# Kernel tuning notes

Hardware: AMD Instinct MI355X
Metric: run time of the kernel (lower is better)

## Reference

```python
import jax, jax.numpy as jnp
import numpy as np

K = 8            # top-k experts per token
GUMBEL_TAU = 1.0 # training-time gumbel noise scale
ROUTER_TEMP = 1.0
SELECT_TEMP = None  # None -> use ROUTER_TEMP for selection
NORM_PROBS = True
T, D, E = 16384, 4096, 128


def setup_inputs() -> dict:
    key = jax.random.key(0)
    k1, k2 = jax.random.split(key)
    h = jax.random.normal(k1, (T, D), dtype=jnp.float32)
    W = jax.random.normal(k2, (D, E), dtype=jnp.float32) * 0.02  # linear gate params
    token_mask = jnp.ones((T,), dtype=bool)
    return {"h": h, "W": W, "token_mask": token_mask}


def reference(h, W, token_mask):
    # compute_logits: linear gate [T,d] @ [d,E] -> [T,E]
    logits_clean = jnp.einsum('td,de->te', h, W)

    t_sel = SELECT_TEMP if SELECT_TEMP is not None else ROUTER_TEMP
    logits_sel = logits_clean / jnp.maximum(t_sel, 1e-06)

    # training path: add gumbel noise (inference=False, gumbel_tau > 0)
    k_gumbel = jax.random.fold_in(jax.random.key(7), 1)
    uniform = jax.random.uniform(k_gumbel, logits_sel.shape, minval=1e-06, maxval=1 - 1e-06)
    gumbel = -jnp.log(-jnp.log(uniform))
    logits_sel = logits_sel + GUMBEL_TAU * gumbel

    logits_sel = jnp.where(token_mask[:, None], logits_sel, -jnp.inf)

    _, top_indices = jax.lax.top_k(logits_sel, K)  # [T, K]
    mask_full = jax.nn.one_hot(top_indices, E).sum(axis=1).astype(bool)  # [T, E]
    mask_full = mask_full & token_mask[:, None]

    t_mix = jnp.maximum(ROUTER_TEMP, 1e-06)
    probs = jax.nn.softmax(logits_clean / t_mix, axis=-1)
    probs = jnp.where(token_mask[:, None], probs, 0.0)

    if NORM_PROBS:
        masked_probs = jnp.where(mask_full, probs, 0.0)
        denom = jnp.maximum(masked_probs.sum(axis=-1, keepdims=True), 1e-09)
        probs = masked_probs / denom
        probs = jnp.where(token_mask[:, None], probs, 0.0)

    return (mask_full, probs, logits_clean, logits_sel)
```

## Files before the change

kernel.cpp:

```cpp
#include <hip/hip_runtime.h>
#include <stdint.h>

#define T_TOK 16384
#define D_DIM 4096
#define E_EXP 128
#define TE ((size_t)T_TOK * E_EXP)

#define TAU 3e-4f
#define FLAG_CAP 8192
#define WT_OFF 65536
#define WT_ELEMS ((size_t)E_EXP * D_DIM)

#define NSPLIT 2
#define KLEN (D_DIM / NSPLIT)
#define BMg 128
#define BKg 64

typedef __attribute__((ext_vector_type(8))) short short8;
typedef __attribute__((ext_vector_type(4))) float f32x4;

#define TF_ROUND(x0, x1, r) { x0 += x1; x1 = (x1 << r) | (x1 >> (32 - r)); x1 ^= x0; }

__host__ __device__ inline void tf2x32(uint32_t k0, uint32_t k1, uint32_t x0, uint32_t x1,
                                       uint32_t* o0, uint32_t* o1) {
  uint32_t ks2 = k0 ^ k1 ^ 0x1BD11BDAu;
  x0 += k0; x1 += k1;
  TF_ROUND(x0, x1, 13) TF_ROUND(x0, x1, 15) TF_ROUND(x0, x1, 26) TF_ROUND(x0, x1, 6)
  x0 += k1; x1 += ks2 + 1u;
  TF_ROUND(x0, x1, 17) TF_ROUND(x0, x1, 29) TF_ROUND(x0, x1, 16) TF_ROUND(x0, x1, 24)
  x0 += ks2; x1 += k0 + 2u;
  TF_ROUND(x0, x1, 13) TF_ROUND(x0, x1, 15) TF_ROUND(x0, x1, 26) TF_ROUND(x0, x1, 6)
  x0 += k0; x1 += k1 + 3u;
  TF_ROUND(x0, x1, 17) TF_ROUND(x0, x1, 29) TF_ROUND(x0, x1, 16) TF_ROUND(x0, x1, 24)
  x0 += k1; x1 += ks2 + 4u;
  TF_ROUND(x0, x1, 13) TF_ROUND(x0, x1, 15) TF_ROUND(x0, x1, 26) TF_ROUND(x0, x1, 6)
  x0 += ks2; x1 += k0 + 5u;
  *o0 = x0; *o1 = x1;
}

__device__ inline uint32_t rng_bits(uint32_t j, uint32_t fk0, uint32_t fk1) {
  uint32_t o0, o1;
  tf2x32(fk0, fk1, 0u, j, &o0, &o1);
  return o0 ^ o1;
}

__device__ inline float gumbel_f32(uint32_t j, uint32_t fk0, uint32_t fk1) {
  uint32_t bits = rng_bits(j, fk0, fk1);
  float f = __uint_as_float((bits >> 9) | 0x3f800000u) - 1.0f;
  const float mn = 1e-6f;
  const float mx = (float)(1.0 - 1e-6);
  float u = fmaxf(mn, f * (mx - mn) + mn);
  float nl = -logf(u);
  return -__logf(nl);
}

__device__ inline double gumbel_f64(uint32_t j, uint32_t fk0, uint32_t fk1) {
  uint32_t bits = rng_bits(j, fk0, fk1);
  float f = __uint_as_float((bits >> 9) | 0x3f800000u) - 1.0f;
  const float mn = 1e-6f;
  const float mx = (float)(1.0 - 1e-6);
  float u = fmaxf(mn, f * (mx - mn) + mn);
  return -log(-log((double)u));
}

__device__ inline unsigned short f2bf(float x) {
  uint32_t u = __float_as_uint(x);
  return (unsigned short)((u + 0x7fffu + ((u >> 16) & 1u)) >> 16);
}
__device__ inline float bf2f(unsigned short h) { return __uint_as_float(((uint32_t)h) << 16); }

__device__ __forceinline__ void gload_lds16(const unsigned short* g, unsigned short* l) {
  __builtin_amdgcn_global_load_lds(
      (const __attribute__((address_space(1))) unsigned int*)g,
      (__attribute__((address_space(3))) unsigned int*)l, 16, 0, 0);
}

__global__ __launch_bounds__(256) void prep_kernel(const float* __restrict__ W,
                                                   unsigned short* __restrict__ WFhi,
                                                   unsigned short* __restrict__ WFlo,
                                                   int* __restrict__ wsi) {
  if (blockIdx.x == 0 && threadIdx.x < 16) wsi[threadIdx.x] = 0;
  const int gslot = blockIdx.x * 256 + threadIdx.x;
  const int kb  = gslot >> 9;
  const int rem = gslot & 511;
  const int cg  = rem >> 6;
  const int ln  = rem & 63;
  const int q = ln >> 4, m = ln & 15;
  const int e  = cg * 16 + m;
  const int k0 = kb * 32 + q * 8;

  __attribute__((aligned(16))) unsigned short hi[8];
  __attribute__((aligned(16))) unsigned short lo[8];
  #pragma unroll
  for (int j = 0; j < 8; j++) {
    float w = W[(size_t)(k0 + j) * E_EXP + e];
    unsigned short h16 = f2bf(w);
    hi[j] = h16;
    lo[j] = f2bf(w - bf2f(h16));
  }
  *(uint4*)(WFhi + (size_t)gslot * 8) = *(const uint4*)hi;
  *(uint4*)(WFlo + (size_t)gslot * 8) = *(const uint4*)lo;
}

__global__ __launch_bounds__(512, 2) void gemm_mfma(const float* __restrict__ h,
                                                    const unsigned short* __restrict__ WFhi,
                                                    const unsigned short* __restrict__ WFlo,
                                                    float* __restrict__ outbase) {
  __shared__ __align__(16) unsigned short sAhi[2][8192];
  __shared__ __align__(16) unsigned short sAlo[2][8192];
  __shared__ __align__(16) unsigned short sBhi[2][8192];
  __shared__ __align__(16) unsigned short sBlo[2][8192];

  const int tid  = threadIdx.x;
  const int ln   = tid & 63;
  const int wv   = tid >> 6;
  const int m    = ln & 15;
  const int quad = ln >> 4;
  const int rh   = wv >> 2;
  const int ch   = wv & 3;
  const int t0   = blockIdx.x * BMg;
  const int kbase = blockIdx.y * KLEN;

  const float* asrc = h + (size_t)(t0 + wv * 16 + m) * D_DIM + kbase + quad * 8;

  const size_t gslot8 = (size_t)tid * 8;
  unsigned short* bdst_h[2][2] = {{ &sBhi[0][wv * 512], &sBhi[0][4096 + wv * 512] },
                                  { &sBhi[1][wv * 512], &sBhi[1][4096 + wv * 512] }};
  unsigned short* bdst_l[2][2] = {{ &sBlo[0][wv * 512], &sBlo[0][4096 + wv * 512] },
                                  { &sBlo[1][wv * 512], &sBlo[1][4096 + wv * 512] }};

  f32x4 acc[4][2];
  #pragma unroll
  for (int r = 0; r < 4; r++)
    #pragma unroll
    for (int c = 0; c < 2; c++) acc[r][c] = (f32x4){0.f, 0.f, 0.f, 0.f};

  {
    const size_t boff = ((size_t)(kbase >> 5)) * 4096;
    gload_lds16(WFhi + boff + gslot8,        bdst_h[0][0]);
    gload_lds16(WFhi + boff + 4096 + gslot8, bdst_h[0][1]);
    gload_lds16(WFlo + boff + gslot8,        bdst_l[0][0]);
    gload_lds16(WFlo + boff + 4096 + gslot8, bdst_l[0][1]);

    float4 a0 = *(const float4*)(asrc);
    float4 a1 = *(const float4*)(asrc + 4);
    float4 a2 = *(const float4*)(asrc + 32);
    float4 a3 = *(const float4*)(asrc + 36);
    float v0[8] = {a0.x, a0.y, a0.z, a0.w, a1.x, a1.y, a1.z, a1.w};
    float v1[8] = {a2.x, a2.y, a2.z, a2.w, a3.x, a3.y, a3.z, a3.w};
    __attribute__((aligned(16))) unsigned short h0[8], l0[8], h1[8], l1[8];
    #pragma unroll
    for (int j = 0; j < 8; j++) {
      unsigned short t16 = f2bf(v0[j]); h0[j] = t16; l0[j] = f2bf(v0[j] - bf2f(t16));
      t16 = f2bf(v1[j]);                h1[j] = t16; l1[j] = f2bf(v1[j] - bf2f(t16));
    }
    *(uint4*)&sAhi[0][(size_t)tid * 8]         = *(const uint4*)h0;
    *(uint4*)&sAlo[0][(size_t)tid * 8]         = *(const uint4*)l0;
    *(uint4*)&sAhi[0][(size_t)(tid + 512) * 8] = *(const uint4*)h1;
    *(uint4*)&sAlo[0][(size_t)(tid + 512) * 8] = *(const uint4*)l1;
    __syncthreads();
  }

  int cur = 0;
  for (int k0 = 0; k0 < KLEN; k0 += BKg) {
    const int kn  = k0 + BKg;
    const bool nxt = (kn < KLEN);
    float4 a0, a1, a2, a3;

    if (nxt) {
      const int nb = cur ^ 1;
      const size_t boff = ((size_t)((kbase + kn) >> 5)) * 4096;
      gload_lds16(WFhi + boff + gslot8,        bdst_h[nb][0]);
      gload_lds16(WFhi + boff + 4096 + gslot8, bdst_h[nb][1]);
      gload_lds16(WFlo + boff + gslot8,        bdst_l[nb][0]);
      gload_lds16(WFlo + boff + 4096 + gslot8, bdst_l[nb][1]);
      a0 = *(const float4*)(asrc + kn);
      a1 = *(const float4*)(asrc + kn + 4);
      a2 = *(const float4*)(asrc + kn + 32);
      a3 = *(const float4*)(asrc + kn + 36);
    }

    short8 ahi[4][2], alo[4][2], bhi[2][2], blo[2][2];
    #pragma unroll
    for (int ks = 0; ks < 2; ks++) {
      #pragma unroll
      for (int r = 0; r < 4; r++) {
        const int slot = (ks * 512 + (rh * 4 + r) * 64 + ln) * 8;
        ahi[r][ks] = *(const short8*)&sAhi[cur][slot];
        alo[r][ks] = *(const short8*)&sAlo[cur][slot];
      }
      #pragma unroll
      for (int c = 0; c < 2; c++) {
        const int slot = (ks * 512 + (ch * 2 + c) * 64 + ln) * 8;
        bhi[c][ks] = *(const short8*)&sBhi[cur][slot];
        blo[c][ks] = *(const short8*)&sBlo[cur][slot];
      }
    }
    #pragma unroll
    for (int ks = 0; ks < 2; ks++)
      #pragma unroll
      for (int r = 0; r < 4; r++)
        #pragma unroll
        for (int c = 0; c < 2; c++) {
          acc[r][c] = __builtin_amdgcn_mfma_f32_16x16x32_bf16(ahi[r][ks], bhi[c][ks], acc[r][c], 0, 0, 0);
          acc[r][c] = __builtin_amdgcn_mfma_f32_16x16x32_bf16(ahi[r][ks], blo[c][ks], acc[r][c], 0, 0, 0);
          acc[r][c] = __builtin_amdgcn_mfma_f32_16x16x32_bf16(alo[r][ks], bhi[c][ks], acc[r][c], 0, 0, 0);
        }

    if (nxt) {
      const int nb = cur ^ 1;
      float v0[8] = {a0.x, a0.y, a0.z, a0.w, a1.x, a1.y, a1.z, a1.w};
      float v1[8] = {a2.x, a2.y, a2.z, a2.w, a3.x, a3.y, a3.z, a3.w};
      __attribute__((aligned(16))) unsigned short h0[8], l0[8], h1[8], l1[8];
      #pragma unroll
      for (int j = 0; j < 8; j++) {
        unsigned short t16 = f2bf(v0[j]); h0[j] = t16; l0[j] = f2bf(v0[j] - bf2f(t16));
        t16 = f2bf(v1[j]);                h1[j] = t16; l1[j] = f2bf(v1[j] - bf2f(t16));
      }
      *(uint4*)&sAhi[nb][(size_t)tid * 8]         = *(const uint4*)h0;
      *(uint4*)&sAlo[nb][(size_t)tid * 8]         = *(const uint4*)l0;
      *(uint4*)&sAhi[nb][(size_t)(tid + 512) * 8] = *(const uint4*)h1;
      *(uint4*)&sAlo[nb][(size_t)(tid + 512) * 8] = *(const uint4*)l1;
    }
    __syncthreads();
    cur ^= 1;
  }

  float* ob = outbase + (size_t)blockIdx.y * TE;
  #pragma unroll
  for (int r = 0; r < 4; r++)
    #pragma unroll
    for (int c = 0; c < 2; c++) {
      const int e = ch * 32 + 16 * c + m;
      #pragma unroll
      for (int reg = 0; reg < 4; reg++) {
        const int t = t0 + rh * 64 + 16 * r + 4 * quad + reg;
        ob[(size_t)t * E_EXP + e] = acc[r][c][reg];
      }
    }
}

__device__ inline uint32_t ordkey(float v) {
  uint32_t b = __float_as_uint(v);
  return (b & 0x80000000u) ? ~b : (b | 0x80000000u);
}
__device__ inline float inv_ordkey(uint32_t k) {
  return (k & 0x80000000u) ? __uint_as_float(k & 0x7fffffffu) : __uint_as_float(~k);
}
__device__ inline uint32_t wave_max_u32(uint32_t v) {
  #pragma unroll
  for (int off = 32; off > 0; off >>= 1) {
    uint32_t o = __shfl_xor(v, off, 64);
    v = (o > v) ? o : v;
  }
  return v;
}
__device__ inline unsigned long long wave_max_u64(unsigned long long v) {
  #pragma unroll
  for (int off = 32; off > 0; off >>= 1) {
    unsigned long long o = __shfl_xor(v, off, 64);
    v = (o > v) ? o : v;
  }
  return v;
}
__device__ inline float wave_max_f32(float v) {
  #pragma unroll
  for (int off = 32; off > 0; off >>= 1) v = fmaxf(v, __shfl_xor(v, off, 64));
  return v;
}
__device__ inline float wave_sum_f32(float v) {
  #pragma unroll
  for (int off = 32; off > 0; off >>= 1) v += __shfl_xor(v, off, 64);
  return v;
}
__device__ inline double wave_sum_f64(double v) {
  #pragma unroll
  for (int off = 32; off > 0; off >>= 1) v += __shfl_xor(v, off, 64);
  return v;
}

__global__ __launch_bounds__(256) void route_kernel(float* out,
                                                    int* flag_cnt, int* flags,
                                                    uint32_t fk0, uint32_t fk1) {
  const int lane = threadIdx.x & 63;
  const int t = blockIdx.x * 4 + (threadIdx.x >> 6);
  const size_t base = (size_t)t * E_EXP;
  float* mask_o   = out;
  float* probs_o  = out + TE;
  float* lclean_o = out + 2 * TE;
  float* lsel_o   = out + 3 * TE;

  double a0 = 0.0, a1 = 0.0;
  #pragma unroll
  for (int s = 0; s < NSPLIT; s++) {
    a0 += (double)out[(size_t)s * TE + base + lane];
    a1 += (double)out[(size_t)s * TE + base + lane + 64];
  }
  const float lc0 = (float)a0, lc1 = (float)a1;

  const float ls0 = lc0 + gumbel_f32((uint32_t)(base + lane), fk0, fk1);
  const float ls1 = lc1 + gumbel_f32((uint32_t)(base + lane + 64), fk0, fk1);

  const uint32_t key0 = ordkey(ls0);
  const uint32_t key1 = ordkey(ls1);
  bool sel0 = false, sel1 = false;
  uint32_t w8 = 0;
  #pragma unroll
  for (int it = 0; it < 8; ++it) {
    uint32_t k0v = sel0 ? 0u : key0;
    uint32_t k1v = sel1 ? 0u : key1;
    w8 = wave_max_u32(k0v > k1v ? k0v : k1v);
    unsigned long long b0 = __ballot(k0v == w8);
    if (b0) {
      if (lane == __ffsll(b0) - 1) sel0 = true;
    } else {
      unsigned long long b1 = __ballot(k1v == w8);
      if (lane == __ffsll(b1) - 1) sel1 = true;
    }
  }
  {
    uint32_t k0v = sel0 ? 0u : key0;
    uint32_t k1v = sel1 ? 0u : key1;
    uint32_t w9 = wave_max_u32(k0v > k1v ? k0v : k1v);
    float gap = inv_ordkey(w8) - inv_ordkey(w9);
    if (lane == 0 && gap < TAU) {
      int idx = atomicAdd(flag_cnt, 1);
      if (idx < FLAG_CAP) flags[idx] = t;
    }
  }

  float mx = wave_max_f32(fmaxf(lc0, lc1));
  float p0 = __expf(lc0 - mx);
  float p1 = __expf(lc1 - mx);
  float s8 = wave_sum_f32((sel0 ? p0 : 0.f) + (sel1 ? p1 : 0.f));

  lclean_o[base + lane]       = lc0;
  lclean_o[base + lane + 64]  = lc1;
  lsel_o[base + lane]         = ls0;
  lsel_o[base + lane + 64]    = ls1;
  mask_o[base + lane]         = sel0 ? 1.0f : 0.0f;
  mask_o[base + lane + 64]    = sel1 ? 1.0f : 0.0f;
  probs_o[base + lane]        = sel0 ? (p0 / s8) : 0.0f;
  probs_o[base + lane + 64]   = sel1 ? (p1 / s8) : 0.0f;
}

__global__ __launch_bounds__(256) void recompute_kernel(const float* __restrict__ h,
                                                        const float* __restrict__ W,
                                                        const int* __restrict__ flag_cnt,
                                                        const int* __restrict__ flags,
                                                        float* __restrict__ mask_out,
                                                        float* __restrict__ probs_out,
                                                        float* __restrict__ lclean_out,
                                                        float* __restrict__ lsel_out,
                                                        uint32_t fk0, uint32_t fk1) {
  __shared__ __align__(16) float shf[D_DIM];
  __shared__ double dsum[E_EXP];
  __shared__ float larr[E_EXP];
  const int tid = threadIdx.x;
  int cnt = *flag_cnt;
  if (cnt > FLAG_CAP) cnt = FLAG_CAP;

  for (int ii = blockIdx.x; ii < cnt; ii += gridDim.x) {
    const int t = flags[ii];
    #pragma unroll
    for (int s = 0; s < 4; s++) {
      int f4 = s * 256 + tid;
      *(float4*)&shf[f4 * 4] = *(const float4*)(h + (size_t)t * D_DIM + f4 * 4);
    }
    __syncthreads();

    const int e = tid & 127;
    const int half = tid >> 7;
    const int kb = half * (D_DIM / 2);
    double acc[8];
    #pragma unroll
    for (int j = 0; j < 8; j++) acc[j] = 0.0;
    #pragma unroll 2
    for (int k = 0; k < D_DIM / 2; k += 8) {
      #pragma unroll
      for (int j = 0; j < 8; j++) {
        int kk = kb + k + j;
        acc[j] = fma((double)shf[kk], (double)W[(size_t)kk * E_EXP + e], acc[j]);
      }
    }
    double a = ((acc[0] + acc[1]) + (acc[2] + acc[3])) + ((acc[4] + acc[5]) + (acc[6] + acc[7]));
    if (half == 1) dsum[e] = a;
    __syncthreads();
    if (half == 0) {
      float lc = (float)(a + dsum[e]);
      larr[e] = lc;
      lclean_out[(size_t)t * E_EXP + e] = lc;
    }
    __syncthreads();

    if (tid < 64) {
      const size_t base = (size_t)t * E_EXP;
      const int lane = tid;
      float lc0 = larr[lane], lc1 = larr[lane + 64];
      float ls0 = lc0 + (float)gumbel_f64((uint32_t)(base + lane), fk0, fk1);
      float ls1 = lc1 + (float)gumbel_f64((uint32_t)(base + lane + 64), fk0, fk1);
      lsel_out[base + lane]      = ls0;
      lsel_out[base + lane + 64] = ls1;

      unsigned long long pk0 = (((unsigned long long)ordkey(ls0)) << 32) | (unsigned)(127 - lane);
      unsigned long long pk1 = (((unsigned long long)ordkey(ls1)) << 32) | (unsigned)(63 - lane);
      bool sel0 = false, sel1 = false;
      #pragma unroll
      for (int it = 0; it < 8; ++it) {
        unsigned long long cc0 = sel0 ? 0ull : pk0;
        unsigned long long cc1 = sel1 ? 0ull : pk1;
        unsigned long long mm = wave_max_u64(cc0 > cc1 ? cc0 : cc1);
        int ew = 127 - (int)(mm & 0xffull);
        if (ew == lane)      sel0 = true;
        if (ew == lane + 64) sel1 = true;
      }
      float mx = wave_max_f32(fmaxf(lc0, lc1));
      double pd0 = exp((double)lc0 - (double)mx);
      double pd1 = exp((double)lc1 - (double)mx);
      double s8 = wave_sum_f64((sel0 ? pd0 : 0.0) + (sel1 ? pd1 : 0.0));

      mask_out[base + lane]       = sel0 ? 1.0f : 0.0f;
      mask_out[base + lane + 64]  = sel1 ? 1.0f : 0.0f;
      probs_out[base + lane]      = sel0 ? (float)(pd0 / s8) : 0.0f;
      probs_out[base + lane + 64] = sel1 ? (float)(pd1 / s8) : 0.0f;
    }
    __syncthreads();
  }
}

extern "C" void kernel_launch(void* const* d_in, const int* in_sizes, int n_in,
                              void* d_out, int out_size, void* d_ws, size_t ws_size,
                              hipStream_t stream) {
  const float* h = (const float*)d_in[0];
  const float* W = (const float*)d_in[1];

  float* out      = (float*)d_out;
  float* mask_o   = out;
  float* probs_o  = out + TE;
  float* lclean_o = out + 2 * TE;
  float* lsel_o   = out + 3 * TE;

  int* wsi   = (int*)d_ws;
  int* flags = wsi + 16;
  unsigned short* WFhi = (unsigned short*)((char*)d_ws + WT_OFF);
  unsigned short* WFlo = WFhi + WT_ELEMS;

  uint32_t fk0, fk1;
  tf2x32(0u, 7u, 0u, 1u, &fk0, &fk1);

  prep_kernel<<<256, 256, 0, stream>>>(W, WFhi, WFlo, wsi);
  gemm_mfma<<<dim3(T_TOK / BMg, NSPLIT), 512, 0, stream>>>(h, WFhi, WFlo, out);
  route_kernel<<<T_TOK / 4, 256, 0, stream>>>(out, wsi, flags, fk0, fk1);
  recompute_kernel<<<256, 256, 0, stream>>>(h, W, wsi, flags, mask_o, probs_o, lclean_o, lsel_o,
                                            fk0, fk1);
}
```

Before: 488.2 us.

## Deepen GEMM pipeline with two-stage A register prefetch and partial waitcnt barriers

Restructures the GEMM main loop into a manually unrolled two-iteration software pipeline. Global loads of A are issued two K-steps ahead into alternating register sets, while B tiles are copied directly into LDS. Barriers use explicit s_waitcnt vmcnt(4) so outstanding A loads can stay in flight across a barrier, and sched_barrier fences keep the compiler from reordering the issue stages. This aims to hide global memory latency behind the MFMA compute, at the cost of more live registers and correctness that depends on the exact count of outstanding loads.

```diff
diff --git a/kernel.cpp b/kernel.cpp
--- a/kernel.cpp
+++ b/kernel.cpp
@@ -102,6 +102,76 @@
   *(uint4*)(WFlo + (size_t)gslot * 8) = *(const uint4*)lo;
 }
 
+#define GEMM_ISSUE_B(KK, NB) do {                                          \
+    const size_t boff_ = ((size_t)((kbase + (KK)) >> 5)) * 4096;           \
+    gload_lds16(WFhi + boff_ + gslot8,        bdst_h[NB][0]);              \
+    gload_lds16(WFhi + boff_ + 4096 + gslot8, bdst_h[NB][1]);              \
+    gload_lds16(WFlo + boff_ + gslot8,        bdst_l[NB][0]);              \
+    gload_lds16(WFlo + boff_ + 4096 + gslot8, bdst_l[NB][1]);              \
+  } while (0)
+
+#define GEMM_LOAD_A(KK, S) do {                                            \
+    S##_0 = *(const float4*)(asrc + (KK));                                 \
+    S##_1 = *(const float4*)(asrc + (KK) + 4);                             \
+    S##_2 = *(const float4*)(asrc + (KK) + 32);                            \
+    S##_3 = *(const float4*)(asrc + (KK) + 36);                            \
+  } while (0)
+
+#define GEMM_CONV_A(S, NB) do {                                            \
+    float v0_[8] = {S##_0.x, S##_0.y, S##_0.z, S##_0.w,                    \
+                    S##_1.x, S##_1.y, S##_1.z, S##_1.w};                   \
+    float v1_[8] = {S##_2.x, S##_2.y, S##_2.z, S##_2.w,                    \
+                    S##_3.x, S##_3.y, S##_3.z, S##_3.w};                   \
+    __attribute__((aligned(16))) unsigned short h0_[8], l0_[8], h1_[8], l1_[8]; \
+    _Pragma("unroll")                                                      \
+    for (int j = 0; j < 8; j++) {                                          \
+      unsigned short t16 = f2bf(v0_[j]); h0_[j] = t16; l0_[j] = f2bf(v0_[j] - bf2f(t16)); \
+      t16 = f2bf(v1_[j]);                h1_[j] = t16; l1_[j] = f2bf(v1_[j] - bf2f(t16)); \
+    }                                                                      \
+    *(uint4*)&sAhi[NB][(size_t)tid * 8]         = *(const uint4*)h0_;      \
+    *(uint4*)&sAlo[NB][(size_t)tid * 8]         = *(const uint4*)l0_;      \
+    *(uint4*)&sAhi[NB][(size_t)(tid + 512) * 8] = *(const uint4*)h1_;      \
+    *(uint4*)&sAlo[NB][(size_t)(tid + 512) * 8] = *(const uint4*)l1_;      \
+  } while (0)
+
+#define GEMM_COMPUTE(P) do {                                               \
+    short8 ahi_[4][2], alo_[4][2], bhi_[2][2], blo_[2][2];                 \
+    _Pragma("unroll")                                                      \
+    for (int ks = 0; ks < 2; ks++) {                                       \
+      _Pragma("unroll")                                                    \
+      for (int r = 0; r < 4; r++) {                                        \
+        const int slot_ = (ks * 512 + (rh * 4 + r) * 64 + ln) * 8;         \
+        ahi_[r][ks] = *(const short8*)&sAhi[P][slot_];                     \
+        alo_[r][ks] = *(const short8*)&sAlo[P][slot_];                     \
+      }                                                                    \
+      _Pragma("unroll")                                                    \
+      for (int c = 0; c < 2; c++) {                                        \
+        const int slot_ = (ks * 512 + (ch * 2 + c) * 64 + ln) * 8;         \
+        bhi_[c][ks] = *(const short8*)&sBhi[P][slot_];                     \
+        blo_[c][ks] = *(const short8*)&sBlo[P][slot_];                     \
+      }                                                                    \
+    }                                                                      \
+    _Pragma("unroll")                                                      \
+    for (int ks = 0; ks < 2; ks++)                                         \
+      _Pragma("unroll")                                                    \
+      for (int r = 0; r < 4; r++)                                          \
+        _Pragma("unroll")                                                  \
+        for (int c = 0; c < 2; c++) {                                      \
+          acc[r][c] = __builtin_amdgcn_mfma_f32_16x16x32_bf16(ahi_[r][ks], bhi_[c][ks], acc[r][c], 0, 0, 0); \
+          acc[r][c] = __builtin_amdgcn_mfma_f32_16x16x32_bf16(ahi_[r][ks], blo_[c][ks], acc[r][c], 0, 0, 0); \
+          acc[r][c] = __builtin_amdgcn_mfma_f32_16x16x32_bf16(alo_[r][ks], bhi_[c][ks], acc[r][c], 0, 0, 0); \
+        }                                                                  \
+  } while (0)
+
+#define GEMM_BAR4() do {                                                   \
+    asm volatile("s_waitcnt vmcnt(4) lgkmcnt(0)" ::: "memory");            \
+    __builtin_amdgcn_s_barrier();                                          \
+  } while (0)
+#define GEMM_BAR0() do {                                                   \
+    asm volatile("s_waitcnt vmcnt(0) lgkmcnt(0)" ::: "memory");            \
+    __builtin_amdgcn_s_barrier();                                          \
+  } while (0)
+
 __global__ __launch_bounds__(512, 2) void gemm_mfma(const float* __restrict__ h,
                                                     const unsigned short* __restrict__ WFhi,
                                                     const unsigned short* __restrict__ WFlo,
@@ -135,96 +205,36 @@
     #pragma unroll
     for (int c = 0; c < 2; c++) acc[r][c] = (f32x4){0.f, 0.f, 0.f, 0.f};
 
-  {
-    const size_t boff = ((size_t)(kbase >> 5)) * 4096;
-    gload_lds16(WFhi + boff + gslot8,        bdst_h[0][0]);
-    gload_lds16(WFhi + boff + 4096 + gslot8, bdst_h[0][1]);
-    gload_lds16(WFlo + boff + gslot8,        bdst_l[0][0]);
-    gload_lds16(WFlo + boff + 4096 + gslot8, bdst_l[0][1]);
-
-    float4 a0 = *(const float4*)(asrc);
-    float4 a1 = *(const float4*)(asrc + 4);
-    float4 a2 = *(const float4*)(asrc + 32);
-    float4 a3 = *(const float4*)(asrc + 36);
-    float v0[8] = {a0.x, a0.y, a0.z, a0.w, a1.x, a1.y, a1.z, a1.w};
-    float v1[8] = {a2.x, a2.y, a2.z, a2.w, a3.x, a3.y, a3.z, a3.w};
-    __attribute__((aligned(16))) unsigned short h0[8], l0[8], h1[8], l1[8];
-    #pragma unroll
-    for (int j = 0; j < 8; j++) {
-      unsigned short t16 = f2bf(v0[j]); h0[j] = t16; l0[j] = f2bf(v0[j] - bf2f(t16));
-      t16 = f2bf(v1[j]);                h1[j] = t16; l1[j] = f2bf(v1[j] - bf2f(t16));
-    }
-    *(uint4*)&sAhi[0][(size_t)tid * 8]         = *(const uint4*)h0;
-    *(uint4*)&sAlo[0][(size_t)tid * 8]         = *(const uint4*)l0;
-    *(uint4*)&sAhi[0][(size_t)(tid + 512) * 8] = *(const uint4*)h1;
-    *(uint4*)&sAlo[0][(size_t)(tid + 512) * 8] = *(const uint4*)l1;
-    __syncthreads();
-  }
-
-  int cur = 0;
-  for (int k0 = 0; k0 < KLEN; k0 += BKg) {
-    const int kn  = k0 + BKg;
-    const bool nxt = (kn < KLEN);
-    float4 a0, a1, a2, a3;
-
-    if (nxt) {
-      const int nb = cur ^ 1;
-      const size_t boff = ((size_t)((kbase + kn) >> 5)) * 4096;
-      gload_lds16(WFhi + boff + gslot8,        bdst_h[nb][0]);
-      gload_lds16(WFhi + boff + 4096 + gslot8, bdst_h[nb][1]);
-      gload_lds16(WFlo + boff + gslot8,        bdst_l[nb][0]);
-      gload_lds16(WFlo + boff + 4096 + gslot8, bdst_l[nb][1]);
-      a0 = *(const float4*)(asrc + kn);
-      a1 = *(const float4*)(asrc + kn + 4);
-      a2 = *(const float4*)(asrc + kn + 32);
-      a3 = *(const float4*)(asrc + kn + 36);
-    }
-
-    short8 ahi[4][2], alo[4][2], bhi[2][2], blo[2][2];
-    #pragma unroll
-    for (int ks = 0; ks < 2; ks++) {
-      #pragma unroll
-      for (int r = 0; r < 4; r++) {
-        const int slot = (ks * 512 + (rh * 4 + r) * 64 + ln) * 8;
-        ahi[r][ks] = *(const short8*)&sAhi[cur][slot];
-        alo[r][ks] = *(const short8*)&sAlo[cur][slot];
-      }
-      #pragma unroll
-      for (int c = 0; c < 2; c++) {
-        const int slot = (ks * 512 + (ch * 2 + c) * 64 + ln) * 8;
-        bhi[c][ks] = *(const short8*)&sBhi[cur][slot];
-        blo[c][ks] = *(const short8*)&sBlo[cur][slot];
-      }
-    }
-    #pragma unroll
-    for (int ks = 0; ks < 2; ks++)
-      #pragma unroll
-      for (int r = 0; r < 4; r++)
-        #pragma unroll
-        for (int c = 0; c < 2; c++) {
-          acc[r][c] = __builtin_amdgcn_mfma_f32_16x16x32_bf16(ahi[r][ks], bhi[c][ks], acc[r][c], 0, 0, 0);
-          acc[r][c] = __builtin_amdgcn_mfma_f32_16x16x32_bf16(ahi[r][ks], blo[c][ks], acc[r][c], 0, 0, 0);
-          acc[r][c] = __builtin_amdgcn_mfma_f32_16x16x32_bf16(alo[r][ks], bhi[c][ks], acc[r][c], 0, 0, 0);
-        }
-
-    if (nxt) {
-      const int nb = cur ^ 1;
-      float v0[8] = {a0.x, a0.y, a0.z, a0.w, a1.x, a1.y, a1.z, a1.w};
-      float v1[8] = {a2.x, a2.y, a2.z, a2.w, a3.x, a3.y, a3.z, a3.w};
-      __attribute__((aligned(16))) unsigned short h0[8], l0[8], h1[8], l1[8];
-      #pragma unroll
-      for (int j = 0; j < 8; j++) {
-        unsigned short t16 = f2bf(v0[j]); h0[j] = t16; l0[j] = f2bf(v0[j] - bf2f(t16));
-        t16 = f2bf(v1[j]);                h1[j] = t16; l1[j] = f2bf(v1[j] - bf2f(t16));
-      }
-      *(uint4*)&sAhi[nb][(size_t)tid * 8]         = *(const uint4*)h0;
-      *(uint4*)&sAlo[nb][(size_t)tid * 8]         = *(const uint4*)l0;
-      *(uint4*)&sAhi[nb][(size_t)(tid + 512) * 8] = *(const uint4*)h1;
-      *(uint4*)&sAlo[nb][(size_t)(tid + 512) * 8] = *(const uint4*)l1;
-    }
-    __syncthreads();
-    cur ^= 1;
-  }
+  float4 a0_0, a0_1, a0_2, a0_3;
+  float4 a1_0, a1_1, a1_2, a1_3;
+
+  GEMM_LOAD_A(0, a0);
+  GEMM_ISSUE_B(0, 0);
+  GEMM_CONV_A(a0, 0);
+  __builtin_amdgcn_sched_barrier(0);
+  GEMM_LOAD_A(BKg, a1);
+  GEMM_BAR4();
+
+  for (int kk = 0; kk < KLEN - 2 * BKg; kk += 2 * BKg) {
+    GEMM_ISSUE_B(kk + BKg, 1);
+    __builtin_amdgcn_sched_barrier(0);
+    GEMM_LOAD_A(kk + 2 * BKg, a0);
+    GEMM_COMPUTE(0);
+    GEMM_CONV_A(a1, 1);
+    GEMM_BAR4();
+    GEMM_ISSUE_B(kk + 2 * BKg, 0);
+    __builtin_amdgcn_sched_barrier(0);
+    GEMM_LOAD_A(kk + 3 * BKg, a1);
+    GEMM_COMPUTE(1);
+    GEMM_CONV_A(a0, 0);
+    GEMM_BAR4();
+  }
+
+  GEMM_ISSUE_B(KLEN - BKg, 1);
+  GEMM_COMPUTE(0);
+  GEMM_CONV_A(a1, 1);
+  GEMM_BAR0();
+  GEMM_COMPUTE(1);
 
   float* ob = outbase + (size_t)blockIdx.y * TE;
   #pragma unroll
```

Measured after the change: 496.1 us. Within noise of the previous version (+1.6%).
